# Performance work log

Hardware: AMD Instinct MI355X
Metric: run time of the kernel (lower is better)

Reference implementation:

```python
import jax, jax.numpy as jnp
import numpy as np

N = 1_500_000
CB, CT, CO, B = 96, 128, 96, 8
BN_EPS = 1e-5


def setup_inputs() -> dict:
    key = jax.random.key(0)
    k1, k2, k3, k4 = jax.random.split(key, 4)
    return {
        "backbone_F": jax.random.normal(k1, (N, CB), dtype=jnp.float32),
        "batch_idx": jax.random.randint(k2, (N,), 0, B, dtype=jnp.int32),
        "text_feats": jax.random.normal(k3, (B, CT), dtype=jnp.float32),
        "W": jax.random.normal(k4, (CB + CT, CO), dtype=jnp.float32) * (1.0 / np.sqrt(CB + CT)),
        "gamma": jnp.ones((CO,), dtype=jnp.float32),
        "beta": jnp.zeros((CO,), dtype=jnp.float32),
    }


def reference(backbone_F, batch_idx, text_feats, W, gamma, beta):
    # gather text feats per point via batch index: [N, CT]
    rep_text = text_feats[batch_idx]
    # concat backbone + text feats: [N, CB+CT]
    combined = jnp.concatenate([backbone_F, rep_text], axis=1)
    # 1x1 sparse conv == pointwise GEMM (no bias): [N, CO]
    x = combined @ W
    # BatchNorm (training mode: batch stats over the N points)
    mean = jnp.mean(x, axis=0)
    var = jnp.var(x, axis=0)
    x = (x - mean) * jax.lax.rsqrt(var + BN_EPS) * gamma + beta
    # ReLU
    return jnp.maximum(x, 0.0)
```

## Files before the change

### kernel.cpp

```cpp
#include <hip/hip_runtime.h>
#include <hip/hip_bf16.h>

#define N_PTS 1500000
#define NT_TILES (N_PTS / 16)
#define CBCH 96
#define CTCH 128
#define COCH 96
#define NB 8
#define BN_EPS 1e-5f
#define GRID1 512
#define STPAD 100

#define GSUM_OFF 0
#define GSQ_OFF 96
#define T_OFF 384

typedef __attribute__((ext_vector_type(8))) short bf16x8;
typedef __attribute__((ext_vector_type(4))) float f32x4;

__device__ __forceinline__ short f2bf(float f) {
    __hip_bfloat16 h = __float2bfloat16(f);
    short s;
    __builtin_memcpy(&s, &h, sizeof(s));
    return s;
}

__global__ void k0_init(const float* __restrict__ text, const float* __restrict__ W,
                        float* __restrict__ ws) {
    if (blockIdx.x == NB) {
        for (int i = threadIdx.x; i < 192; i += blockDim.x) ws[i] = 0.f;
        return;
    }
    int b = blockIdx.x;
    int c = threadIdx.x;
    if (c < COCH) {
        float acc = 0.f;
        #pragma unroll 8
        for (int k = 0; k < CTCH; ++k)
            acc += text[b * CTCH + k] * W[(CBCH + k) * COCH + c];
        ws[T_OFF + b * COCH + c] = acc;
    }
}


__device__ __forceinline__ void stage_W(const float* __restrict__ W, short* sW) {
    for (int i = threadIdx.x; i < CBCH * COCH; i += blockDim.x) {
        int k = i / COCH, c = i % COCH;
        int ct = c >> 4, lr = c & 15;
        int kt = k >> 5, grp = (k >> 3) & 3, j = k & 7;
        sW[(((ct * 3 + kt) * 64) + (grp * 16 + lr)) * 8 + j] = f2bf(W[i]);
    }
}

__device__ __forceinline__ void load_bfrag_lds(const short* sW, int lane, bf16x8 bf[6][3]) {
    #pragma unroll
    for (int ct = 0; ct < 6; ++ct)
        #pragma unroll
        for (int kt = 0; kt < 3; ++kt)
            bf[ct][kt] = *reinterpret_cast<const bf16x8*>(sW + ((ct * 3 + kt) * 64 + lane) * 8);
}

__device__ __forceinline__ void tile_acc(const float* __restrict__ bb,
                                         const int* __restrict__ bidx,
                                         const float* __restrict__ sT,
                                         const bf16x8 bf[6][3],
                                         int base, int grp, int lr,
                                         f32x4 acc[6]) {
    int b = bidx[base + lr];
    #pragma unroll
    for (int ct = 0; ct < 6; ++ct)
        acc[ct] = *reinterpret_cast<const f32x4*>(&sT[b * STPAD + ct * 16 + grp * 4]);

    bf16x8 pf[3];
    #pragma unroll
    for (int kt = 0; kt < 3; ++kt) {
        const f32x4* p = reinterpret_cast<const f32x4*>(bb + (size_t)(base + lr) * CBCH + kt * 32 + grp * 8);
        f32x4 x0 = p[0], x1 = p[1];
        #pragma unroll
        for (int j = 0; j < 4; ++j) {
            pf[kt][j]     = f2bf(x0[j]);
            pf[kt][4 + j] = f2bf(x1[j]);
        }
    }
    #pragma unroll
    for (int ct = 0; ct < 6; ++ct)
        #pragma unroll
        for (int kt = 0; kt < 3; ++kt)
            acc[ct] = __builtin_amdgcn_mfma_f32_16x16x32_bf16(bf[ct][kt], pf[kt], acc[ct], 0, 0, 0);
}

__global__ __launch_bounds__(256, 2) void k1_stats(const float* __restrict__ bb,
                                                   const int* __restrict__ bidx,
                                                   const float* __restrict__ W,
                                                   float* __restrict__ ws) {
    __shared__ __align__(16) short sW[6 * 3 * 64 * 8];
    __shared__ __align__(16) float sT[NB * STPAD];
    __shared__ float sredS[4][COCH];
    __shared__ float sredQ[4][COCH];

    stage_W(W, sW);
    for (int i = threadIdx.x; i < NB * COCH; i += blockDim.x)
        sT[(i / COCH) * STPAD + (i % COCH)] = ws[T_OFF + i];
    __syncthreads();

    const int lane = threadIdx.x & 63;
    const int wv = threadIdx.x >> 6;
    const int grp = lane >> 4, lr = lane & 15;

    bf16x8 bf[6][3];
    load_bfrag_lds(sW, lane, bf);

    f32x4 sum[6], sq[6];
    #pragma unroll
    for (int ct = 0; ct < 6; ++ct) { sum[ct] = (f32x4)0.f; sq[ct] = (f32x4)0.f; }

    const int gw = blockIdx.x * 4 + wv;
    for (int t = gw; t < NT_TILES; t += GRID1 * 4) {
        int base = t * 16;
        f32x4 acc[6];
        tile_acc(bb, bidx, sT, bf, base, grp, lr, acc);
        #pragma unroll
        for (int ct = 0; ct < 6; ++ct) {
            sum[ct] += acc[ct];
            sq[ct] += acc[ct] * acc[ct];
        }
    }

    #pragma unroll
    for (int ct = 0; ct < 6; ++ct)
        #pragma unroll
        for (int r = 0; r < 4; ++r) {
            float s = sum[ct][r], q = sq[ct][r];
            s += __shfl_xor(s, 1);  q += __shfl_xor(q, 1);
            s += __shfl_xor(s, 2);  q += __shfl_xor(q, 2);
            s += __shfl_xor(s, 4);  q += __shfl_xor(q, 4);
            s += __shfl_xor(s, 8);  q += __shfl_xor(q, 8);
            if (lr == 0) {
                sredS[wv][ct * 16 + grp * 4 + r] = s;
                sredQ[wv][ct * 16 + grp * 4 + r] = q;
            }
        }
    __syncthreads();
    if (threadIdx.x < COCH) {
        int c = threadIdx.x;
        atomicAdd(&ws[GSUM_OFF + c], sredS[0][c] + sredS[1][c] + sredS[2][c] + sredS[3][c]);
        atomicAdd(&ws[GSQ_OFF + c],  sredQ[0][c] + sredQ[1][c] + sredQ[2][c] + sredQ[3][c]);
    }
}

__global__ __launch_bounds__(256, 2) void k3_out(const float* __restrict__ bb,
                                                 const int* __restrict__ bidx,
                                                 const float* __restrict__ W,
                                                 const float* __restrict__ gamma,
                                                 const float* __restrict__ beta,
                                                 const float* __restrict__ ws,
                                                 float* __restrict__ out) {
    __shared__ __align__(16) short sW[6 * 3 * 64 * 8];
    __shared__ __align__(16) float sT[NB * STPAD];
    __shared__ __align__(16) float sScale[COCH];
    __shared__ __align__(16) float sBias[COCH];

    stage_W(W, sW);
    for (int i = threadIdx.x; i < NB * COCH; i += blockDim.x)
        sT[(i / COCH) * STPAD + (i % COCH)] = ws[T_OFF + i];
    if (threadIdx.x < COCH) {
        int c = threadIdx.x;
        float mean = ws[GSUM_OFF + c] * (1.f / (float)N_PTS);
        float var  = ws[GSQ_OFF + c] * (1.f / (float)N_PTS) - mean * mean;
        float scl  = gamma[c] * rsqrtf(var + BN_EPS);
        sScale[c] = scl;
        sBias[c]  = beta[c] - mean * scl;
    }
    __syncthreads();

    const int lane = threadIdx.x & 63;
    const int wv = threadIdx.x >> 6;
    const int grp = lane >> 4, lr = lane & 15;

    bf16x8 bf[6][3];
    load_bfrag_lds(sW, lane, bf);

    f32x4 sc[6], bs[6];
    #pragma unroll
    for (int ct = 0; ct < 6; ++ct) {
        sc[ct] = *reinterpret_cast<const f32x4*>(&sScale[ct * 16 + grp * 4]);
        bs[ct] = *reinterpret_cast<const f32x4*>(&sBias[ct * 16 + grp * 4]);
    }

    const int gw = blockIdx.x * 4 + wv;
    for (int t = NT_TILES - 1 - gw; t >= 0; t -= GRID1 * 4) {
        int base = t * 16;
        f32x4 acc[6];
        tile_acc(bb, bidx, sT, bf, base, grp, lr, acc);
        #pragma unroll
        for (int ct = 0; ct < 6; ++ct) {
            f32x4 y;
            #pragma unroll
            for (int r = 0; r < 4; ++r)
                y[r] = fmaxf(acc[ct][r] * sc[ct][r] + bs[ct][r], 0.f);
            __builtin_nontemporal_store(y,
                reinterpret_cast<f32x4*>(out + (size_t)(base + lr) * COCH + ct * 16 + grp * 4));
        }
    }
}

extern "C" void kernel_launch(void* const* d_in, const int* in_sizes, int n_in,
                              void* d_out, int out_size, void* d_ws, size_t ws_size,
                              hipStream_t stream) {
    const float* bb    = (const float*)d_in[0];
    const int*   bidx  = (const int*)d_in[1];
    const float* text  = (const float*)d_in[2];
    const float* W     = (const float*)d_in[3];
    const float* gamma = (const float*)d_in[4];
    const float* beta  = (const float*)d_in[5];
    float* out = (float*)d_out;
    float* ws  = (float*)d_ws;

    hipLaunchKernelGGL(k0_init, dim3(NB + 1), dim3(128), 0, stream, text, W, ws);
    hipLaunchKernelGGL(k1_stats, dim3(GRID1), dim3(256), 0, stream, bb, bidx, W, ws);
    hipLaunchKernelGGL(k3_out, dim3(GRID1), dim3(256), 0, stream, bb, bidx, W, gamma, beta, ws, out);
}
```

Measured before the change: 369.3 us.

## Fuse stats and output kernels with a grid-wide atomic barrier

Merges the statistics pass and the output pass into one persistent kernel that synchronises all blocks through an atomic counter barrier in the workspace. Each block now computes the text-projection table itself instead of reading it from a separate init kernel. Second-pass loads of the backbone now use nontemporal hints. This removes two kernel launches and the per-block restaging of weights, at the cost of redundant text projection per block and a deadlock risk if all 512 blocks cannot be co-resident.

```diff
diff --git a/kernel.cpp b/kernel.cpp
--- a/kernel.cpp
+++ b/kernel.cpp
@@ -9,11 +9,12 @@
 #define NB 8
 #define BN_EPS 1e-5f
 #define GRID1 512
+#define NWAVE (GRID1 * 4)
 #define STPAD 100
 
 #define GSUM_OFF 0
 #define GSQ_OFF 96
-#define T_OFF 384
+#define BAR_OFF 192
 
 typedef __attribute__((ext_vector_type(8))) short bf16x8;
 typedef __attribute__((ext_vector_type(4))) float f32x4;
@@ -25,21 +26,8 @@
     return s;
 }
 
-__global__ void k0_init(const float* __restrict__ text, const float* __restrict__ W,
-                        float* __restrict__ ws) {
-    if (blockIdx.x == NB) {
-        for (int i = threadIdx.x; i < 192; i += blockDim.x) ws[i] = 0.f;
-        return;
-    }
-    int b = blockIdx.x;
-    int c = threadIdx.x;
-    if (c < COCH) {
-        float acc = 0.f;
-        #pragma unroll 8
-        for (int k = 0; k < CTCH; ++k)
-            acc += text[b * CTCH + k] * W[(CBCH + k) * COCH + c];
-        ws[T_OFF + b * COCH + c] = acc;
-    }
+__global__ void k0z(float* __restrict__ ws) {
+    if (threadIdx.x < 256) ws[threadIdx.x] = 0.f;
 }
 
 
@@ -60,6 +48,7 @@
             bf[ct][kt] = *reinterpret_cast<const bf16x8*>(sW + ((ct * 3 + kt) * 64 + lane) * 8);
 }
 
+template <bool NTLOAD>
 __device__ __forceinline__ void tile_acc(const float* __restrict__ bb,
                                          const int* __restrict__ bidx,
                                          const float* __restrict__ sT,
@@ -75,7 +64,9 @@
     #pragma unroll
     for (int kt = 0; kt < 3; ++kt) {
         const f32x4* p = reinterpret_cast<const f32x4*>(bb + (size_t)(base + lr) * CBCH + kt * 32 + grp * 8);
-        f32x4 x0 = p[0], x1 = p[1];
+        f32x4 x0, x1;
+        if (NTLOAD) { x0 = __builtin_nontemporal_load(p); x1 = __builtin_nontemporal_load(p + 1); }
+        else        { x0 = p[0]; x1 = p[1]; }
         #pragma unroll
         for (int j = 0; j < 4; ++j) {
             pf[kt][j]     = f2bf(x0[j]);
@@ -89,18 +80,30 @@
             acc[ct] = __builtin_amdgcn_mfma_f32_16x16x32_bf16(bf[ct][kt], pf[kt], acc[ct], 0, 0, 0);
 }
 
-__global__ __launch_bounds__(256, 2) void k1_stats(const float* __restrict__ bb,
-                                                   const int* __restrict__ bidx,
-                                                   const float* __restrict__ W,
-                                                   float* __restrict__ ws) {
+__global__ __launch_bounds__(256, 2) void fused(const float* __restrict__ bb,
+                                                const int* __restrict__ bidx,
+                                                const float* __restrict__ text,
+                                                const float* __restrict__ W,
+                                                const float* __restrict__ gamma,
+                                                const float* __restrict__ beta,
+                                                float* __restrict__ ws,
+                                                float* __restrict__ out) {
     __shared__ __align__(16) short sW[6 * 3 * 64 * 8];
     __shared__ __align__(16) float sT[NB * STPAD];
     __shared__ float sredS[4][COCH];
     __shared__ float sredQ[4][COCH];
+    __shared__ __align__(16) float sScale[COCH];
+    __shared__ __align__(16) float sBias[COCH];
 
     stage_W(W, sW);
-    for (int i = threadIdx.x; i < NB * COCH; i += blockDim.x)
-        sT[(i / COCH) * STPAD + (i % COCH)] = ws[T_OFF + i];
+    for (int i = threadIdx.x; i < NB * COCH; i += blockDim.x) {
+        int b = i / COCH, c = i % COCH;
+        float acc = 0.f;
+        #pragma unroll 8
+        for (int k = 0; k < CTCH; ++k)
+            acc += text[b * CTCH + k] * W[(CBCH + k) * COCH + c];
+        sT[b * STPAD + c] = acc;
+    }
     __syncthreads();
 
     const int lane = threadIdx.x & 63;
@@ -110,76 +113,65 @@
     bf16x8 bf[6][3];
     load_bfrag_lds(sW, lane, bf);
 
-    f32x4 sum[6], sq[6];
-    #pragma unroll
-    for (int ct = 0; ct < 6; ++ct) { sum[ct] = (f32x4)0.f; sq[ct] = (f32x4)0.f; }
-
     const int gw = blockIdx.x * 4 + wv;
-    for (int t = gw; t < NT_TILES; t += GRID1 * 4) {
-        int base = t * 16;
-        f32x4 acc[6];
-        tile_acc(bb, bidx, sT, bf, base, grp, lr, acc);
-        #pragma unroll
-        for (int ct = 0; ct < 6; ++ct) {
-            sum[ct] += acc[ct];
-            sq[ct] += acc[ct] * acc[ct];
-        }
-    }
-
-    #pragma unroll
-    for (int ct = 0; ct < 6; ++ct)
-        #pragma unroll
-        for (int r = 0; r < 4; ++r) {
-            float s = sum[ct][r], q = sq[ct][r];
-            s += __shfl_xor(s, 1);  q += __shfl_xor(q, 1);
-            s += __shfl_xor(s, 2);  q += __shfl_xor(q, 2);
-            s += __shfl_xor(s, 4);  q += __shfl_xor(q, 4);
-            s += __shfl_xor(s, 8);  q += __shfl_xor(q, 8);
-            if (lr == 0) {
-                sredS[wv][ct * 16 + grp * 4 + r] = s;
-                sredQ[wv][ct * 16 + grp * 4 + r] = q;
+
+    {
+        f32x4 sum[6], sq[6];
+        #pragma unroll
+        for (int ct = 0; ct < 6; ++ct) { sum[ct] = (f32x4)0.f; sq[ct] = (f32x4)0.f; }
+
+        for (int t = gw; t < NT_TILES; t += NWAVE) {
+            int base = t * 16;
+            f32x4 acc[6];
+            tile_acc<false>(bb, bidx, sT, bf, base, grp, lr, acc);
+            #pragma unroll
+            for (int ct = 0; ct < 6; ++ct) {
+                sum[ct] += acc[ct];
+                sq[ct] += acc[ct] * acc[ct];
             }
         }
-    __syncthreads();
+        #pragma unroll
+        for (int ct = 0; ct < 6; ++ct)
+            #pragma unroll
+            for (int r = 0; r < 4; ++r) {
+                float s = sum[ct][r], q = sq[ct][r];
+                s += __shfl_xor(s, 1);  q += __shfl_xor(q, 1);
+                s += __shfl_xor(s, 2);  q += __shfl_xor(q, 2);
+                s += __shfl_xor(s, 4);  q += __shfl_xor(q, 4);
+                s += __shfl_xor(s, 8);  q += __shfl_xor(q, 8);
+                if (lr == 0) {
+                    sredS[wv][ct * 16 + grp * 4 + r] = s;
+                    sredQ[wv][ct * 16 + grp * 4 + r] = q;
+                }
+            }
+        __syncthreads();
+        if (threadIdx.x < COCH) {
+            int c = threadIdx.x;
+            atomicAdd(&ws[GSUM_OFF + c], sredS[0][c] + sredS[1][c] + sredS[2][c] + sredS[3][c]);
+            atomicAdd(&ws[GSQ_OFF + c],  sredQ[0][c] + sredQ[1][c] + sredQ[2][c] + sredQ[3][c]);
+        }
+    }
+
+    __syncthreads();
+    if (threadIdx.x == 0) {
+        int* bar = (int*)&ws[BAR_OFF];
+        __hip_atomic_fetch_add(bar, 1, __ATOMIC_ACQ_REL, __HIP_MEMORY_SCOPE_AGENT);
+        while (__hip_atomic_load(bar, __ATOMIC_ACQUIRE, __HIP_MEMORY_SCOPE_AGENT) < GRID1) {}
+    }
+    __syncthreads();
+
     if (threadIdx.x < COCH) {
         int c = threadIdx.x;
-        atomicAdd(&ws[GSUM_OFF + c], sredS[0][c] + sredS[1][c] + sredS[2][c] + sredS[3][c]);
-        atomicAdd(&ws[GSQ_OFF + c],  sredQ[0][c] + sredQ[1][c] + sredQ[2][c] + sredQ[3][c]);
-    }
-}
-
-__global__ __launch_bounds__(256, 2) void k3_out(const float* __restrict__ bb,
-                                                 const int* __restrict__ bidx,
-                                                 const float* __restrict__ W,
-                                                 const float* __restrict__ gamma,
-                                                 const float* __restrict__ beta,
-                                                 const float* __restrict__ ws,
-                                                 float* __restrict__ out) {
-    __shared__ __align__(16) short sW[6 * 3 * 64 * 8];
-    __shared__ __align__(16) float sT[NB * STPAD];
-    __shared__ __align__(16) float sScale[COCH];
-    __shared__ __align__(16) float sBias[COCH];
-
-    stage_W(W, sW);
-    for (int i = threadIdx.x; i < NB * COCH; i += blockDim.x)
-        sT[(i / COCH) * STPAD + (i % COCH)] = ws[T_OFF + i];
-    if (threadIdx.x < COCH) {
-        int c = threadIdx.x;
-        float mean = ws[GSUM_OFF + c] * (1.f / (float)N_PTS);
-        float var  = ws[GSQ_OFF + c] * (1.f / (float)N_PTS) - mean * mean;
+        float s = __hip_atomic_load(&ws[GSUM_OFF + c], __ATOMIC_RELAXED, __HIP_MEMORY_SCOPE_AGENT);
+        float q = __hip_atomic_load(&ws[GSQ_OFF + c],  __ATOMIC_RELAXED, __HIP_MEMORY_SCOPE_AGENT);
+        float mean = s * (1.f / (float)N_PTS);
+        float var  = q * (1.f / (float)N_PTS) - mean * mean;
         float scl  = gamma[c] * rsqrtf(var + BN_EPS);
         sScale[c] = scl;
         sBias[c]  = beta[c] - mean * scl;
     }
     __syncthreads();
 
-    const int lane = threadIdx.x & 63;
-    const int wv = threadIdx.x >> 6;
-    const int grp = lane >> 4, lr = lane & 15;
-
-    bf16x8 bf[6][3];
-    load_bfrag_lds(sW, lane, bf);
-
     f32x4 sc[6], bs[6];
     #pragma unroll
     for (int ct = 0; ct < 6; ++ct) {
@@ -187,11 +179,10 @@
         bs[ct] = *reinterpret_cast<const f32x4*>(&sBias[ct * 16 + grp * 4]);
     }
 
-    const int gw = blockIdx.x * 4 + wv;
-    for (int t = NT_TILES - 1 - gw; t >= 0; t -= GRID1 * 4) {
+    for (int t = NT_TILES - 1 - gw; t >= 0; t -= NWAVE) {
         int base = t * 16;
         f32x4 acc[6];
-        tile_acc(bb, bidx, sT, bf, base, grp, lr, acc);
+        tile_acc<true>(bb, bidx, sT, bf, base, grp, lr, acc);
         #pragma unroll
         for (int ct = 0; ct < 6; ++ct) {
             f32x4 y;
@@ -216,7 +207,7 @@
     float* out = (float*)d_out;
     float* ws  = (float*)d_ws;
 
-    hipLaunchKernelGGL(k0_init, dim3(NB + 1), dim3(128), 0, stream, text, W, ws);
-    hipLaunchKernelGGL(k1_stats, dim3(GRID1), dim3(256), 0, stream, bb, bidx, W, ws);
-    hipLaunchKernelGGL(k3_out, dim3(GRID1), dim3(256), 0, stream, bb, bidx, W, gamma, beta, ws, out);
-}
+    hipLaunchKernelGGL(k0z, dim3(1), dim3(256), 0, stream, ws);
+    hipLaunchKernelGGL(fused, dim3(GRID1), dim3(256), 0, stream,
+                       bb, bidx, text, W, gamma, beta, ws, out);
+}
```

Result: slower. 444.6 us (+20.4%).

## Split output channels across wave halves and compute text projection per block

Applied to the files above, without the earlier changes.

Each block now has 8 waves: two groups of four that share the same point tiles, with each group computing half of the 96 output channels. The grid doubles to 1024 blocks, so register pressure per wave drops (3x3 B-fragments instead of 6x3) and more waves are in flight. The text projection (text @ W_text) is now recomputed inside every block instead of being precomputed by a separate kernel, and the first kernel only zeroes the stats. In exchange, every backbone row is loaded twice (once by each half, though the second load may hit cache), and each block repeats a small GEMV in its prologue.

```diff
diff --git a/kernel.cpp b/kernel.cpp
--- a/kernel.cpp
+++ b/kernel.cpp
@@ -8,12 +8,12 @@
 #define COCH 96
 #define NB 8
 #define BN_EPS 1e-5f
-#define GRID1 512
+#define GRID1 1024
+#define NSTREAM (GRID1 * 4)
 #define STPAD 100
 
 #define GSUM_OFF 0
 #define GSQ_OFF 96
-#define T_OFF 384
 
 typedef __attribute__((ext_vector_type(8))) short bf16x8;
 typedef __attribute__((ext_vector_type(4))) float f32x4;
@@ -25,21 +25,8 @@
     return s;
 }
 
-__global__ void k0_init(const float* __restrict__ text, const float* __restrict__ W,
-                        float* __restrict__ ws) {
-    if (blockIdx.x == NB) {
-        for (int i = threadIdx.x; i < 192; i += blockDim.x) ws[i] = 0.f;
-        return;
-    }
-    int b = blockIdx.x;
-    int c = threadIdx.x;
-    if (c < COCH) {
-        float acc = 0.f;
-        #pragma unroll 8
-        for (int k = 0; k < CTCH; ++k)
-            acc += text[b * CTCH + k] * W[(CBCH + k) * COCH + c];
-        ws[T_OFF + b * COCH + c] = acc;
-    }
+__global__ void k0z(float* __restrict__ ws) {
+    if (threadIdx.x < 192) ws[threadIdx.x] = 0.f;
 }
 
 
@@ -52,24 +39,26 @@
     }
 }
 
-__device__ __forceinline__ void load_bfrag_lds(const short* sW, int lane, bf16x8 bf[6][3]) {
-    #pragma unroll
-    for (int ct = 0; ct < 6; ++ct)
+__device__ __forceinline__ void load_bfrag_half(const short* sW, int lane, int half,
+                                                bf16x8 bf[3][3]) {
+    #pragma unroll
+    for (int ct = 0; ct < 3; ++ct)
         #pragma unroll
         for (int kt = 0; kt < 3; ++kt)
-            bf[ct][kt] = *reinterpret_cast<const bf16x8*>(sW + ((ct * 3 + kt) * 64 + lane) * 8);
-}
-
-__device__ __forceinline__ void tile_acc(const float* __restrict__ bb,
-                                         const int* __restrict__ bidx,
-                                         const float* __restrict__ sT,
-                                         const bf16x8 bf[6][3],
-                                         int base, int grp, int lr,
-                                         f32x4 acc[6]) {
+            bf[ct][kt] = *reinterpret_cast<const bf16x8*>(
+                sW + (((half * 3 + ct) * 3 + kt) * 64 + lane) * 8);
+}
+
+__device__ __forceinline__ void tile_acc_half(const float* __restrict__ bb,
+                                              const int* __restrict__ bidx,
+                                              const float* __restrict__ sT,
+                                              const bf16x8 bf[3][3],
+                                              int base, int half, int grp, int lr,
+                                              f32x4 acc[3]) {
     int b = bidx[base + lr];
     #pragma unroll
-    for (int ct = 0; ct < 6; ++ct)
-        acc[ct] = *reinterpret_cast<const f32x4*>(&sT[b * STPAD + ct * 16 + grp * 4]);
+    for (int ct = 0; ct < 3; ++ct)
+        acc[ct] = *reinterpret_cast<const f32x4*>(&sT[b * STPAD + (half * 3 + ct) * 16 + grp * 4]);
 
     bf16x8 pf[3];
     #pragma unroll
@@ -83,14 +72,15 @@
         }
     }
     #pragma unroll
-    for (int ct = 0; ct < 6; ++ct)
+    for (int ct = 0; ct < 3; ++ct)
         #pragma unroll
         for (int kt = 0; kt < 3; ++kt)
             acc[ct] = __builtin_amdgcn_mfma_f32_16x16x32_bf16(bf[ct][kt], pf[kt], acc[ct], 0, 0, 0);
 }
 
-__global__ __launch_bounds__(256, 2) void k1_stats(const float* __restrict__ bb,
+__global__ __launch_bounds__(512, 2) void k1_stats(const float* __restrict__ bb,
                                                    const int* __restrict__ bidx,
+                                                   const float* __restrict__ text,
                                                    const float* __restrict__ W,
                                                    float* __restrict__ ws) {
     __shared__ __align__(16) short sW[6 * 3 * 64 * 8];
@@ -99,35 +89,42 @@
     __shared__ float sredQ[4][COCH];
 
     stage_W(W, sW);
-    for (int i = threadIdx.x; i < NB * COCH; i += blockDim.x)
-        sT[(i / COCH) * STPAD + (i % COCH)] = ws[T_OFF + i];
+    for (int i = threadIdx.x; i < NB * COCH; i += blockDim.x) {
+        int b = i / COCH, c = i % COCH;
+        float acc = 0.f;
+        #pragma unroll 8
+        for (int k = 0; k < CTCH; ++k)
+            acc += text[b * CTCH + k] * W[(CBCH + k) * COCH + c];
+        sT[b * STPAD + c] = acc;
+    }
     __syncthreads();
 
     const int lane = threadIdx.x & 63;
     const int wv = threadIdx.x >> 6;
+    const int half = wv >> 2;
+    const int stream = wv & 3;
     const int grp = lane >> 4, lr = lane & 15;
 
-    bf16x8 bf[6][3];
-    load_bfrag_lds(sW, lane, bf);
-
-    f32x4 sum[6], sq[6];
-    #pragma unroll
-    for (int ct = 0; ct < 6; ++ct) { sum[ct] = (f32x4)0.f; sq[ct] = (f32x4)0.f; }
-
-    const int gw = blockIdx.x * 4 + wv;
-    for (int t = gw; t < NT_TILES; t += GRID1 * 4) {
+    bf16x8 bf[3][3];
+    load_bfrag_half(sW, lane, half, bf);
+
+    f32x4 sum[3], sq[3];
+    #pragma unroll
+    for (int ct = 0; ct < 3; ++ct) { sum[ct] = (f32x4)0.f; sq[ct] = (f32x4)0.f; }
+
+    for (int t = blockIdx.x * 4 + stream; t < NT_TILES; t += NSTREAM) {
         int base = t * 16;
-        f32x4 acc[6];
-        tile_acc(bb, bidx, sT, bf, base, grp, lr, acc);
-        #pragma unroll
-        for (int ct = 0; ct < 6; ++ct) {
+        f32x4 acc[3];
+        tile_acc_half(bb, bidx, sT, bf, base, half, grp, lr, acc);
+        #pragma unroll
+        for (int ct = 0; ct < 3; ++ct) {
             sum[ct] += acc[ct];
             sq[ct] += acc[ct] * acc[ct];
         }
     }
 
     #pragma unroll
-    for (int ct = 0; ct < 6; ++ct)
+    for (int ct = 0; ct < 3; ++ct)
         #pragma unroll
         for (int r = 0; r < 4; ++r) {
             float s = sum[ct][r], q = sq[ct][r];
@@ -136,8 +133,8 @@
             s += __shfl_xor(s, 4);  q += __shfl_xor(q, 4);
             s += __shfl_xor(s, 8);  q += __shfl_xor(q, 8);
             if (lr == 0) {
-                sredS[wv][ct * 16 + grp * 4 + r] = s;
-                sredQ[wv][ct * 16 + grp * 4 + r] = q;
+                sredS[stream][half * 48 + ct * 16 + grp * 4 + r] = s;
+                sredQ[stream][half * 48 + ct * 16 + grp * 4 + r] = q;
             }
         }
     __syncthreads();
@@ -148,8 +145,9 @@
     }
 }
 
-__global__ __launch_bounds__(256, 2) void k3_out(const float* __restrict__ bb,
+__global__ __launch_bounds__(512, 2) void k3_out(const float* __restrict__ bb,
                                                  const int* __restrict__ bidx,
+                                                 const float* __restrict__ text,
                                                  const float* __restrict__ W,
                                                  const float* __restrict__ gamma,
                                                  const float* __restrict__ beta,
@@ -161,8 +159,14 @@
     __shared__ __align__(16) float sBias[COCH];
 
     stage_W(W, sW);
-    for (int i = threadIdx.x; i < NB * COCH; i += blockDim.x)
-        sT[(i / COCH) * STPAD + (i % COCH)] = ws[T_OFF + i];
+    for (int i = threadIdx.x; i < NB * COCH; i += blockDim.x) {
+        int b = i / COCH, c = i % COCH;
+        float acc = 0.f;
+        #pragma unroll 8
+        for (int k = 0; k < CTCH; ++k)
+            acc += text[b * CTCH + k] * W[(CBCH + k) * COCH + c];
+        sT[b * STPAD + c] = acc;
+    }
     if (threadIdx.x < COCH) {
         int c = threadIdx.x;
         float mean = ws[GSUM_OFF + c] * (1.f / (float)N_PTS);
@@ -175,31 +179,32 @@
 
     const int lane = threadIdx.x & 63;
     const int wv = threadIdx.x >> 6;
+    const int half = wv >> 2;
+    const int stream = wv & 3;
     const int grp = lane >> 4, lr = lane & 15;
 
-    bf16x8 bf[6][3];
-    load_bfrag_lds(sW, lane, bf);
-
-    f32x4 sc[6], bs[6];
-    #pragma unroll
-    for (int ct = 0; ct < 6; ++ct) {
-        sc[ct] = *reinterpret_cast<const f32x4*>(&sScale[ct * 16 + grp * 4]);
-        bs[ct] = *reinterpret_cast<const f32x4*>(&sBias[ct * 16 + grp * 4]);
-    }
-
-    const int gw = blockIdx.x * 4 + wv;
-    for (int t = NT_TILES - 1 - gw; t >= 0; t -= GRID1 * 4) {
+    bf16x8 bf[3][3];
+    load_bfrag_half(sW, lane, half, bf);
+
+    f32x4 sc[3], bs[3];
+    #pragma unroll
+    for (int ct = 0; ct < 3; ++ct) {
+        sc[ct] = *reinterpret_cast<const f32x4*>(&sScale[(half * 3 + ct) * 16 + grp * 4]);
+        bs[ct] = *reinterpret_cast<const f32x4*>(&sBias[(half * 3 + ct) * 16 + grp * 4]);
+    }
+
+    for (int t = NT_TILES - 1 - (blockIdx.x * 4 + stream); t >= 0; t -= NSTREAM) {
         int base = t * 16;
-        f32x4 acc[6];
-        tile_acc(bb, bidx, sT, bf, base, grp, lr, acc);
-        #pragma unroll
-        for (int ct = 0; ct < 6; ++ct) {
+        f32x4 acc[3];
+        tile_acc_half(bb, bidx, sT, bf, base, half, grp, lr, acc);
+        #pragma unroll
+        for (int ct = 0; ct < 3; ++ct) {
             f32x4 y;
             #pragma unroll
             for (int r = 0; r < 4; ++r)
                 y[r] = fmaxf(acc[ct][r] * sc[ct][r] + bs[ct][r], 0.f);
             __builtin_nontemporal_store(y,
-                reinterpret_cast<f32x4*>(out + (size_t)(base + lr) * COCH + ct * 16 + grp * 4));
+                reinterpret_cast<f32x4*>(out + (size_t)(base + lr) * COCH + (half * 3 + ct) * 16 + grp * 4));
         }
     }
 }
@@ -216,7 +221,7 @@
     float* out = (float*)d_out;
     float* ws  = (float*)d_ws;
 
-    hipLaunchKernelGGL(k0_init, dim3(NB + 1), dim3(128), 0, stream, text, W, ws);
-    hipLaunchKernelGGL(k1_stats, dim3(GRID1), dim3(256), 0, stream, bb, bidx, W, ws);
-    hipLaunchKernelGGL(k3_out, dim3(GRID1), dim3(256), 0, stream, bb, bidx, W, gamma, beta, ws, out);
-}
+    hipLaunchKernelGGL(k0z, dim3(1), dim3(256), 0, stream, ws);
+    hipLaunchKernelGGL(k1_stats, dim3(GRID1), dim3(512), 0, stream, bb, bidx, text, W, ws);
+    hipLaunchKernelGGL(k3_out, dim3(GRID1), dim3(512), 0, stream, bb, bidx, text, W, gamma, beta, ws, out);
+}
```

Measured after the change: 517.5 us. 40.1% more time.

## Raise grid size, fold text projection into kernels, coalesce backbone loads

Applied to the files above, without the earlier changes.

Grid grows from 512 to 2048 blocks. The separate text-projection kernel goes away: every block now computes the 8x96 text-times-W table itself in its prologue. The K-permutation of W staging is changed so each lane reads backbone floats at stride 16 (grp*4 with +16 offsets) instead of 32-byte contiguous chunks, which makes wave loads more contiguous across groups. The risk is redundant prologue work: each block does 98k multiply-adds and reads W and text, repeated over 4096 blocks across both kernels.

```diff
diff --git a/kernel.cpp b/kernel.cpp
--- a/kernel.cpp
+++ b/kernel.cpp
@@ -8,12 +8,12 @@
 #define COCH 96
 #define NB 8
 #define BN_EPS 1e-5f
-#define GRID1 512
+#define GRID1 2048
+#define NWAVE (GRID1 * 4)
 #define STPAD 100
 
 #define GSUM_OFF 0
 #define GSQ_OFF 96
-#define T_OFF 384
 
 typedef __attribute__((ext_vector_type(8))) short bf16x8;
 typedef __attribute__((ext_vector_type(4))) float f32x4;
@@ -25,21 +25,8 @@
     return s;
 }
 
-__global__ void k0_init(const float* __restrict__ text, const float* __restrict__ W,
-                        float* __restrict__ ws) {
-    if (blockIdx.x == NB) {
-        for (int i = threadIdx.x; i < 192; i += blockDim.x) ws[i] = 0.f;
-        return;
-    }
-    int b = blockIdx.x;
-    int c = threadIdx.x;
-    if (c < COCH) {
-        float acc = 0.f;
-        #pragma unroll 8
-        for (int k = 0; k < CTCH; ++k)
-            acc += text[b * CTCH + k] * W[(CBCH + k) * COCH + c];
-        ws[T_OFF + b * COCH + c] = acc;
-    }
+__global__ void k0z(float* __restrict__ ws) {
+    if (threadIdx.x < 192) ws[threadIdx.x] = 0.f;
 }
 
 
@@ -47,7 +34,9 @@
     for (int i = threadIdx.x; i < CBCH * COCH; i += blockDim.x) {
         int k = i / COCH, c = i % COCH;
         int ct = c >> 4, lr = c & 15;
-        int kt = k >> 5, grp = (k >> 3) & 3, j = k & 7;
+        int kt = k >> 5, r5 = k & 31;
+        int grp = (r5 & 15) >> 2;
+        int j = (r5 & 3) + ((r5 >> 4) << 2);
         sW[(((ct * 3 + kt) * 64) + (grp * 16 + lr)) * 8 + j] = f2bf(W[i]);
     }
 }
@@ -71,11 +60,12 @@
     for (int ct = 0; ct < 6; ++ct)
         acc[ct] = *reinterpret_cast<const f32x4*>(&sT[b * STPAD + ct * 16 + grp * 4]);
 
+    const f32x4* q = reinterpret_cast<const f32x4*>(bb + (size_t)(base + lr) * CBCH + grp * 4);
     bf16x8 pf[3];
     #pragma unroll
     for (int kt = 0; kt < 3; ++kt) {
-        const f32x4* p = reinterpret_cast<const f32x4*>(bb + (size_t)(base + lr) * CBCH + kt * 32 + grp * 8);
-        f32x4 x0 = p[0], x1 = p[1];
+        f32x4 x0 = q[kt * 8];
+        f32x4 x1 = q[kt * 8 + 4];
         #pragma unroll
         for (int j = 0; j < 4; ++j) {
             pf[kt][j]     = f2bf(x0[j]);
@@ -91,6 +81,7 @@
 
 __global__ __launch_bounds__(256, 2) void k1_stats(const float* __restrict__ bb,
                                                    const int* __restrict__ bidx,
+                                                   const float* __restrict__ text,
                                                    const float* __restrict__ W,
                                                    float* __restrict__ ws) {
     __shared__ __align__(16) short sW[6 * 3 * 64 * 8];
@@ -99,8 +90,14 @@
     __shared__ float sredQ[4][COCH];
 
     stage_W(W, sW);
-    for (int i = threadIdx.x; i < NB * COCH; i += blockDim.x)
-        sT[(i / COCH) * STPAD + (i % COCH)] = ws[T_OFF + i];
+    for (int i = threadIdx.x; i < NB * COCH; i += blockDim.x) {
+        int b = i / COCH, c = i % COCH;
+        float acc = 0.f;
+        #pragma unroll 8
+        for (int k = 0; k < CTCH; ++k)
+            acc += text[b * CTCH + k] * W[(CBCH + k) * COCH + c];
+        sT[b * STPAD + c] = acc;
+    }
     __syncthreads();
 
     const int lane = threadIdx.x & 63;
@@ -115,7 +112,7 @@
     for (int ct = 0; ct < 6; ++ct) { sum[ct] = (f32x4)0.f; sq[ct] = (f32x4)0.f; }
 
     const int gw = blockIdx.x * 4 + wv;
-    for (int t = gw; t < NT_TILES; t += GRID1 * 4) {
+    for (int t = gw; t < NT_TILES; t += NWAVE) {
         int base = t * 16;
         f32x4 acc[6];
         tile_acc(bb, bidx, sT, bf, base, grp, lr, acc);
@@ -150,6 +147,7 @@
 
 __global__ __launch_bounds__(256, 2) void k3_out(const float* __restrict__ bb,
                                                  const int* __restrict__ bidx,
+                                                 const float* __restrict__ text,
                                                  const float* __restrict__ W,
                                                  const float* __restrict__ gamma,
                                                  const float* __restrict__ beta,
@@ -161,8 +159,14 @@
     __shared__ __align__(16) float sBias[COCH];
 
     stage_W(W, sW);
-    for (int i = threadIdx.x; i < NB * COCH; i += blockDim.x)
-        sT[(i / COCH) * STPAD + (i % COCH)] = ws[T_OFF + i];
+    for (int i = threadIdx.x; i < NB * COCH; i += blockDim.x) {
+        int b = i / COCH, c = i % COCH;
+        float acc = 0.f;
+        #pragma unroll 8
+        for (int k = 0; k < CTCH; ++k)
+            acc += text[b * CTCH + k] * W[(CBCH + k) * COCH + c];
+        sT[b * STPAD + c] = acc;
+    }
     if (threadIdx.x < COCH) {
         int c = threadIdx.x;
         float mean = ws[GSUM_OFF + c] * (1.f / (float)N_PTS);
@@ -188,7 +192,7 @@
     }
 
     const int gw = blockIdx.x * 4 + wv;
-    for (int t = NT_TILES - 1 - gw; t >= 0; t -= GRID1 * 4) {
+    for (int t = NT_TILES - 1 - gw; t >= 0; t -= NWAVE) {
         int base = t * 16;
         f32x4 acc[6];
         tile_acc(bb, bidx, sT, bf, base, grp, lr, acc);
@@ -216,7 +220,7 @@
     float* out = (float*)d_out;
     float* ws  = (float*)d_ws;
 
-    hipLaunchKernelGGL(k0_init, dim3(NB + 1), dim3(128), 0, stream, text, W, ws);
-    hipLaunchKernelGGL(k1_stats, dim3(GRID1), dim3(256), 0, stream, bb, bidx, W, ws);
-    hipLaunchKernelGGL(k3_out, dim3(GRID1), dim3(256), 0, stream, bb, bidx, W, gamma, beta, ws, out);
-}
+    hipLaunchKernelGGL(k0z, dim3(1), dim3(256), 0, stream, ws);
+    hipLaunchKernelGGL(k1_stats, dim3(GRID1), dim3(256), 0, stream, bb, bidx, text, W, ws);
+    hipLaunchKernelGGL(k3_out, dim3(GRID1), dim3(256), 0, stream, bb, bidx, text, W, gamma, beta, ws, out);
+}
```

After: 505.1 us. 36.8% more time.
